# Kernel tuning notes

Measured on AMD Instinct MI355X. Metric: run time of the kernel, lower is better.

## Reference

```python
import jax, jax.numpy as jnp
import numpy as np

N_EMBD = 768
HEAD_SIZE = 72
SEQ_LEN = 512
BATCH = 64

def setup_inputs() -> dict:
    key = jax.random.key(0)
    kx, kk, kq, kv = jax.random.split(key, 4)
    # Linear weights stored as [in, out] for x @ W; torch Linear init ~ U(-1/sqrt(in), 1/sqrt(in))
    bound = 1.0 / np.sqrt(N_EMBD)
    x = jax.random.normal(kx, (BATCH, SEQ_LEN, N_EMBD), dtype=jnp.float32)
    Wk = jax.random.uniform(kk, (N_EMBD, HEAD_SIZE), minval=-bound, maxval=bound, dtype=jnp.float32)
    Wq = jax.random.uniform(kq, (N_EMBD, HEAD_SIZE), minval=-bound, maxval=bound, dtype=jnp.float32)
    Wv = jax.random.uniform(kv, (N_EMBD, HEAD_SIZE), minval=-bound, maxval=bound, dtype=jnp.float32)
    return {"x": x, "Wk": Wk, "Wq": Wq, "Wv": Wv}

def reference(x, Wk, Wq, Wv):
    # Single causal self-attention head (dropout in eval mode = identity).
    k = x @ Wk  # [B, T, H]
    q = x @ Wq  # [B, T, H]
    v = x @ Wv  # [B, T, H]
    scale = k.shape[-1] ** (-0.5)
    scores = jnp.einsum('bth,bsh->bts', q, k) * scale  # [B, T, T]
    T = scores.shape[-1]
    causal = jnp.tril(jnp.ones((T, T), dtype=bool))
    scores = jnp.where(causal, scores, -jnp.inf)
    attn = jax.nn.softmax(scores, axis=-1)
    out = jnp.einsum('bts,bsh->bth', attn, v)  # [B, T, H]
    return out
```

## Files before the change

kernel.cpp:

```cpp
#include <hip/hip_runtime.h>


typedef short bf16x8 __attribute__((ext_vector_type(8)));
typedef float f32x4 __attribute__((ext_vector_type(4)));
typedef float f32x4v __attribute__((ext_vector_type(4)));

#define DEVI __device__ __forceinline__

DEVI unsigned f2bf(float f) {
  unsigned u = __builtin_bit_cast(unsigned, f);
  return (u + 0x7fffu + ((u >> 16) & 1u)) >> 16;
}
DEVI unsigned pk2(float a, float b) { return f2bf(a) | (f2bf(b) << 16); }

DEVI void async16(void* lds, const void* g) {
  __builtin_amdgcn_global_load_lds(
      (const __attribute__((address_space(1))) unsigned int*)g,
      (__attribute__((address_space(3))) unsigned int*)lds, 16, 0, 0);
}

__global__ __launch_bounds__(256) void cast_w_k(const float* __restrict__ Wk,
                                                const float* __restrict__ Wq,
                                                const float* __restrict__ Wv,
                                                unsigned short* __restrict__ wbt) {
  __shared__ float ldsT[72][65];
  const int mat = blockIdx.x / 12, kc = blockIdx.x % 12;
  const float* W = (mat == 0) ? Wk : (mat == 1) ? Wq : Wv;
  const float sc = (mat == 1) ? 0.11785113019775793f : 1.0f;
  const float* src = W + kc * 64 * 72;
  for (int i = threadIdx.x; i < 1152; i += 256) {
    float4 d = *(const float4*)(src + i * 4);
    int e = i * 4;
    ldsT[e % 72][e / 72] = d.x;
    ldsT[(e + 1) % 72][(e + 1) / 72] = d.y;
    ldsT[(e + 2) % 72][(e + 2) / 72] = d.z;
    ldsT[(e + 3) % 72][(e + 3) / 72] = d.w;
  }
  __syncthreads();
  for (int c = threadIdx.x; c < 640; c += 256) {
    int h = c >> 3, kb = (c & 7) * 8;
    uint4 o = {0u, 0u, 0u, 0u};
    if (h < 72) {
      const float* rowp = &ldsT[h][kb];
      o.x = pk2(rowp[0] * sc, rowp[1] * sc);
      o.y = pk2(rowp[2] * sc, rowp[3] * sc);
      o.z = pk2(rowp[4] * sc, rowp[5] * sc);
      o.w = pk2(rowp[6] * sc, rowp[7] * sc);
    }
    *(uint4*)(wbt + ((size_t)mat * 80 + h) * 768 + kc * 64 + kb) = o;
  }
}

struct ProjSmem {
  union {
    struct {
      short x[2][64 * 64];
      short w[2][240 * 64];
    } s;
    short t[80 * 72];
  };
};

__global__ __launch_bounds__(256, 2) void proj_k(
    const float* __restrict__ x, const unsigned short* __restrict__ wbt,
    unsigned short* __restrict__ Kg, unsigned short* __restrict__ Qg,
    unsigned short* __restrict__ Vt) {
  __shared__ __align__(16) ProjSmem sm;
  const int row0 = blockIdx.x * 64;
  const int tid = threadIdx.x, wave = tid >> 6, lane = tid & 63;
  const int quad = lane >> 4, l16 = lane & 15;
  const int mg = wave >> 1, ng = wave & 1;
  const int ntile0 = ng * 8, ntn = ng ? 7 : 8;

  const int t0row = tid >> 3, tcb = tid & 7;
  const int wr8 = lane >> 3, wcb = lane & 7;

  f32x4 acc[2][8] = {};

  f32x4v A[2], Bv[2], A2[2], B2[2];

  auto issue_x = [&](int k0, f32x4v* Ar, f32x4v* Br) {
    const float* g0 = x + (size_t)(row0 + t0row) * 768 + k0 + tcb * 8;
    Ar[0] = __builtin_nontemporal_load((const f32x4v*)g0);
    Br[0] = __builtin_nontemporal_load((const f32x4v*)(g0 + 4));
    const float* g1 = g0 + (size_t)32 * 768;
    Ar[1] = __builtin_nontemporal_load((const f32x4v*)g1);
    Br[1] = __builtin_nontemporal_load((const f32x4v*)(g1 + 4));
  };
  auto issue_w = [&](int k0, int nb) {
#pragma unroll
    for (int j = 0; j < 8; ++j) {
      int inst = j * 4 + wave;
      if (inst < 30) {
        int r = inst * 8 + wr8;
        async16(&sm.s.w[nb][inst * 512],
                wbt + (size_t)r * 768 + k0 + ((wcb ^ (r & 7)) * 8));
      }
    }
  };
  auto write_x = [&](int nb, const f32x4v* Ar, const f32x4v* Br) {
    uint4 o0 = {pk2(Ar[0].x, Ar[0].y), pk2(Ar[0].z, Ar[0].w),
                pk2(Br[0].x, Br[0].y), pk2(Br[0].z, Br[0].w)};
    *(uint4*)&sm.s.x[nb][t0row * 64 + ((tcb ^ (t0row & 7)) * 8)] = o0;
    int r1 = t0row + 32;
    uint4 o1 = {pk2(Ar[1].x, Ar[1].y), pk2(Ar[1].z, Ar[1].w),
                pk2(Br[1].x, Br[1].y), pk2(Br[1].z, Br[1].w)};
    *(uint4*)&sm.s.x[nb][r1 * 64 + ((tcb ^ (r1 & 7)) * 8)] = o1;
  };
  auto compute = [&](int cb) {
#pragma unroll
    for (int ks = 0; ks < 2; ++ks) {
      const int pblk = ((ks << 2) | quad) ^ (l16 & 7);
      bf16x8 af[2];
#pragma unroll
      for (int mt = 0; mt < 2; ++mt)
        af[mt] = *(const bf16x8*)&sm.s.x[cb][(mg * 32 + mt * 16 + l16) * 64 + pblk * 8];
#pragma unroll
      for (int j = 0; j < 8; ++j)
        if (j < ntn) {
          int nt = ntile0 + j;
          bf16x8 bfr = *(const bf16x8*)&sm.s.w[cb][(nt * 16 + l16) * 64 + pblk * 8];
          acc[0][j] = __builtin_amdgcn_mfma_f32_16x16x32_bf16(af[0], bfr, acc[0][j], 0, 0, 0);
          acc[1][j] = __builtin_amdgcn_mfma_f32_16x16x32_bf16(af[1], bfr, acc[1][j], 0, 0, 0);
        }
    }
  };

  issue_x(0, A, Bv);
  issue_w(0, 0);
  write_x(0, A, Bv);
  __syncthreads();

  for (int t = 0; t < 11; ++t) {
    const int cur = t & 1;
    if (cur == 0) {
      issue_x((t + 1) * 64, A2, B2);
      issue_w((t + 1) * 64, 1);
      compute(0);
      write_x(1, A2, B2);
    } else {
      issue_x((t + 1) * 64, A, Bv);
      issue_w((t + 1) * 64, 0);
      compute(1);
      write_x(0, A, Bv);
    }
    __syncthreads();
  }
  compute(1);
  __syncthreads();

#pragma unroll
  for (int mt = 0; mt < 2; ++mt)
#pragma unroll
    for (int r = 0; r < 4; ++r) {
      int lrow64 = mg * 32 + mt * 16 + quad * 4 + r;
      size_t grow = (size_t)row0 + lrow64;
#pragma unroll
      for (int j = 0; j < 8; ++j)
        if (j < ntn) {
          int nt = ntile0 + j;
          float v = acc[mt][j][r];
          if (nt < 5) {
            Kg[grow * 104 + nt * 16 + l16] = (unsigned short)f2bf(v);
          } else if (nt < 10) {
            Qg[grow * 104 + (nt - 5) * 16 + l16] = (unsigned short)f2bf(v);
          } else {
            sm.t[((nt - 10) * 16 + l16) * 72 + lrow64] = (short)f2bf(v);
          }
        }
      unsigned short* p = (ng ? Qg : Kg) + grow * 104;
      p[80 + l16] = 0;
      if (l16 < 8) p[96 + l16] = 0;
    }
  __syncthreads();
  int b = blockIdx.x >> 3, t0 = (blockIdx.x & 7) * 64;
  const uint4 ones = {0x3F803F80u, 0x3F803F80u, 0x3F803F80u, 0x3F803F80u};
  for (int c = tid; c < 640; c += 256) {
    int hr = c >> 3, tc = (c & 7) * 8;
    uint4 d = *(const uint4*)&sm.t[hr * 72 + tc];
    if (hr == 72) d = ones;
    *(uint4*)(Vt + ((size_t)b * 80 + hr) * 512 + t0 + tc) = d;
  }
}

__global__ __launch_bounds__(256, 4) void attn_k(
    const unsigned short* __restrict__ Qg, const unsigned short* __restrict__ Kg,
    const unsigned short* __restrict__ Vt, float* __restrict__ out) {
  __shared__ __align__(16) short lk[64 * 104];
  __shared__ __align__(16) short lv[80 * 64];
  __shared__ __align__(16) short lp[4][16 * 72];

  int idx = (blockIdx.x < 256) ? blockIdx.x : 767 - blockIdx.x;
  const int qb = 7 - (idx >> 6), b = idx & 63;
  const int tid = threadIdx.x, wave = tid >> 6, lane = tid & 63;
  const int quad = lane >> 4, l16 = lane & 15;
  const int lrow = lane >> 3, lcb = lane & 7;
  const int trow0 = qb * 64 + wave * 16;

  bf16x8 qf[3];
#pragma unroll
  for (int kt = 0; kt < 3; ++kt)
    qf[kt] = *(const bf16x8*)(Qg + ((size_t)b * 512 + trow0 + l16) * 104 + kt * 32 + quad * 8);

  f32x4 o[5] = {};

  for (int kb = 0; kb <= qb; ++kb) {
    const int s0 = kb * 64;
    const bool diag = (kb == qb);
    const int nact = diag ? (wave + 1) : 4;

#pragma unroll
    for (int j = 0; j < 4; ++j) {
      int inst = j * 4 + wave;
      if (inst < 13)
        async16(&lk[inst * 512], Kg + ((size_t)b * 512 + s0) * 104 + inst * 512 + lane * 8);
    }
    for (int j = wave; j < 10; j += 4) {
      int r = j * 8 + lrow;
      async16(&lv[j * 512], Vt + ((size_t)b * 80 + r) * 512 + s0 + (lcb ^ lrow) * 8);
    }
    __syncthreads();

    f32x4 sacc[4] = {};
#pragma unroll
    for (int kt = 0; kt < 3; ++kt)
      for (int nt = 0; nt < nact; ++nt) {
        bf16x8 kf = *(const bf16x8*)&lk[(nt * 16 + l16) * 104 + kt * 32 + quad * 8];
        sacc[nt] = __builtin_amdgcn_mfma_f32_16x16x32_bf16(qf[kt], kf, sacc[nt], 0, 0, 0);
      }
    if (diag) {
      int nt = wave;
#pragma unroll
      for (int r = 0; r < 4; ++r) {
        int t = trow0 + quad * 4 + r;
        if (s0 + nt * 16 + l16 > t) sacc[nt][r] = -1e30f;
      }
    }
#pragma unroll
    for (int nt = 0; nt < 4; ++nt)
#pragma unroll
      for (int r = 0; r < 4; ++r) {
        float p = (nt < nact) ? __expf(sacc[nt][r]) : 0.0f;
        lp[wave][(quad * 4 + r) * 72 + nt * 16 + l16] = (short)f2bf(p);
      }
#pragma unroll
    for (int ks = 0; ks < 2; ++ks) {
      bf16x8 pf = *(const bf16x8*)&lp[wave][l16 * 72 + ks * 32 + quad * 8];
      const int pblk = ((ks << 2) | quad) ^ (l16 & 7);
#pragma unroll
      for (int nt = 0; nt < 5; ++nt) {
        bf16x8 vf = *(const bf16x8*)&lv[(nt * 16 + l16) * 64 + pblk * 8];
        o[nt] = __builtin_amdgcn_mfma_f32_16x16x32_bf16(pf, vf, o[nt], 0, 0, 0);
      }
    }
    __syncthreads();
  }

#pragma unroll
  for (int r = 0; r < 4; ++r) {
    float l = __shfl(o[4][r], (lane & 48) | 8, 64);
    float inv = 1.0f / l;
    size_t t = (size_t)b * 512 + trow0 + quad * 4 + r;
#pragma unroll
    for (int nt = 0; nt < 5; ++nt) {
      int h = nt * 16 + l16;
      if (h < 72) out[t * 72 + h] = o[nt][r] * inv;
    }
  }
}

extern "C" void kernel_launch(void* const* d_in, const int* in_sizes, int n_in,
                              void* d_out, int out_size, void* d_ws, size_t ws_size,
                              hipStream_t stream) {
  const float* x  = (const float*)d_in[0];
  const float* Wk = (const float*)d_in[1];
  const float* Wq = (const float*)d_in[2];
  const float* Wv = (const float*)d_in[3];
  float* out = (float*)d_out;

  char* ws = (char*)d_ws;
  unsigned short* Kg  = (unsigned short*)(ws);
  unsigned short* Qg  = (unsigned short*)(ws + 6815744);
  unsigned short* Vt  = (unsigned short*)(ws + 13631488);
  unsigned short* wbt = (unsigned short*)(ws + 18874368);

  cast_w_k<<<36, 256, 0, stream>>>(Wk, Wq, Wv, wbt);
  proj_k<<<512, 256, 0, stream>>>(x, wbt, Kg, Qg, Vt);
  attn_k<<<512, 256, 0, stream>>>(Qg, Kg, Vt, out);
}
```

Measured before the change: 188.5 us.

## Double-buffer K/V tiles in attention and deepen projection prefetch with manual waitcnts

The attention kernel now double-buffers its K and V LDS tiles, issuing async loads for the next key block before computing on the current one. This replaces the two full __syncthreads per block with a single explicit waitcnt plus barrier. To fit the doubled shared memory, its launch bounds drop from 4 to 2 blocks per CU. The projection kernel is restructured into an unrolled ping-pong loop with sched_barriers and explicit vmcnt waits, so x loads are prefetched two stages ahead and overlap with MFMA compute. The costs are lower attention occupancy and fragile hand-written wait counts.

```diff
diff --git a/kernel.cpp b/kernel.cpp
--- a/kernel.cpp
+++ b/kernel.cpp
@@ -6,6 +6,7 @@
 typedef float f32x4v __attribute__((ext_vector_type(4)));
 
 #define DEVI __device__ __forceinline__
+#define SB0() __builtin_amdgcn_sched_barrier(0)
 
 DEVI unsigned f2bf(float f) {
   unsigned u = __builtin_bit_cast(unsigned, f);
@@ -77,7 +78,7 @@
 
   f32x4 acc[2][8] = {};
 
-  f32x4v A[2], Bv[2], A2[2], B2[2];
+  f32x4v xa0[2], xb0[2], xa1[2], xb1[2];
 
   auto issue_x = [&](int k0, f32x4v* Ar, f32x4v* Br) {
     const float* g0 = x + (size_t)(row0 + t0row) * 768 + k0 + tcb * 8;
@@ -126,26 +127,44 @@
     }
   };
 
-  issue_x(0, A, Bv);
   issue_w(0, 0);
-  write_x(0, A, Bv);
-  __syncthreads();
-
-  for (int t = 0; t < 11; ++t) {
-    const int cur = t & 1;
-    if (cur == 0) {
-      issue_x((t + 1) * 64, A2, B2);
-      issue_w((t + 1) * 64, 1);
-      compute(0);
-      write_x(1, A2, B2);
-    } else {
-      issue_x((t + 1) * 64, A, Bv);
-      issue_w((t + 1) * 64, 0);
-      compute(1);
-      write_x(0, A, Bv);
-    }
-    __syncthreads();
-  }
+  SB0();
+  issue_x(0, xa0, xb0);
+  write_x(0, xa0, xb0);
+  SB0();
+  issue_x(64, xa1, xb1);
+  SB0();
+  asm volatile("s_waitcnt vmcnt(4) lgkmcnt(0)" ::: "memory");
+  SB0();
+  __builtin_amdgcn_s_barrier();
+
+  for (int t = 0; t < 10; t += 2) {
+    issue_w((t + 1) * 64, 1);
+    SB0();
+    issue_x((t + 2) * 64, xa0, xb0);
+    SB0();
+    compute(0);
+    write_x(1, xa1, xb1);
+    asm volatile("s_waitcnt vmcnt(4) lgkmcnt(0)" ::: "memory");
+    SB0();
+    __builtin_amdgcn_s_barrier();
+    issue_w((t + 2) * 64, 0);
+    SB0();
+    issue_x((t + 3) * 64, xa1, xb1);
+    SB0();
+    compute(1);
+    write_x(0, xa0, xb0);
+    asm volatile("s_waitcnt vmcnt(4) lgkmcnt(0)" ::: "memory");
+    SB0();
+    __builtin_amdgcn_s_barrier();
+  }
+  issue_w(11 * 64, 1);
+  SB0();
+  compute(0);
+  write_x(1, xa1, xb1);
+  asm volatile("s_waitcnt vmcnt(0) lgkmcnt(0)" ::: "memory");
+  SB0();
+  __builtin_amdgcn_s_barrier();
   compute(1);
   __syncthreads();
 
@@ -183,11 +202,11 @@
   }
 }
 
-__global__ __launch_bounds__(256, 4) void attn_k(
+__global__ __launch_bounds__(256, 2) void attn_k(
     const unsigned short* __restrict__ Qg, const unsigned short* __restrict__ Kg,
     const unsigned short* __restrict__ Vt, float* __restrict__ out) {
-  __shared__ __align__(16) short lk[64 * 104];
-  __shared__ __align__(16) short lv[80 * 64];
+  __shared__ __align__(16) short lk[2][64 * 104];
+  __shared__ __align__(16) short lv[2][80 * 64];
   __shared__ __align__(16) short lp[4][16 * 72];
 
   int idx = (blockIdx.x < 256) ? blockIdx.x : 767 - blockIdx.x;
@@ -202,30 +221,41 @@
   for (int kt = 0; kt < 3; ++kt)
     qf[kt] = *(const bf16x8*)(Qg + ((size_t)b * 512 + trow0 + l16) * 104 + kt * 32 + quad * 8);
 
+  auto stage = [&](int kb, int pb) {
+    const int s0 = kb * 64;
+#pragma unroll
+    for (int j = 0; j < 4; ++j) {
+      int inst = j * 4 + wave;
+      if (inst < 13)
+        async16(&lk[pb][inst * 512], Kg + ((size_t)b * 512 + s0) * 104 + inst * 512 + lane * 8);
+    }
+    for (int j = wave; j < 10; j += 4) {
+      int r = j * 8 + lrow;
+      async16(&lv[pb][j * 512], Vt + ((size_t)b * 80 + r) * 512 + s0 + (lcb ^ lrow) * 8);
+    }
+  };
+
   f32x4 o[5] = {};
 
+  stage(0, 0);
+  asm volatile("s_waitcnt vmcnt(0)" ::: "memory");
+  SB0();
+  __builtin_amdgcn_s_barrier();
+
   for (int kb = 0; kb <= qb; ++kb) {
+    const int pb = kb & 1;
     const int s0 = kb * 64;
     const bool diag = (kb == qb);
     const int nact = diag ? (wave + 1) : 4;
 
-#pragma unroll
-    for (int j = 0; j < 4; ++j) {
-      int inst = j * 4 + wave;
-      if (inst < 13)
-        async16(&lk[inst * 512], Kg + ((size_t)b * 512 + s0) * 104 + inst * 512 + lane * 8);
-    }
-    for (int j = wave; j < 10; j += 4) {
-      int r = j * 8 + lrow;
-      async16(&lv[j * 512], Vt + ((size_t)b * 80 + r) * 512 + s0 + (lcb ^ lrow) * 8);
-    }
-    __syncthreads();
+    if (!diag) stage(kb + 1, pb ^ 1);
+    SB0();
 
     f32x4 sacc[4] = {};
 #pragma unroll
     for (int kt = 0; kt < 3; ++kt)
       for (int nt = 0; nt < nact; ++nt) {
-        bf16x8 kf = *(const bf16x8*)&lk[(nt * 16 + l16) * 104 + kt * 32 + quad * 8];
+        bf16x8 kf = *(const bf16x8*)&lk[pb][(nt * 16 + l16) * 104 + kt * 32 + quad * 8];
         sacc[nt] = __builtin_amdgcn_mfma_f32_16x16x32_bf16(qf[kt], kf, sacc[nt], 0, 0, 0);
       }
     if (diag) {
@@ -249,11 +279,15 @@
       const int pblk = ((ks << 2) | quad) ^ (l16 & 7);
 #pragma unroll
       for (int nt = 0; nt < 5; ++nt) {
-        bf16x8 vf = *(const bf16x8*)&lv[(nt * 16 + l16) * 64 + pblk * 8];
+        bf16x8 vf = *(const bf16x8*)&lv[pb][(nt * 16 + l16) * 64 + pblk * 8];
         o[nt] = __builtin_amdgcn_mfma_f32_16x16x32_bf16(pf, vf, o[nt], 0, 0, 0);
       }
     }
-    __syncthreads();
+    if (!diag) {
+      asm volatile("s_waitcnt vmcnt(0) lgkmcnt(0)" ::: "memory");
+      SB0();
+      __builtin_amdgcn_s_barrier();
+    }
   }
 
 #pragma unroll
```

After: 187.2 us (median of 2 runs). No clear change (-0.7%).
